# Kernel tuning notes

Measured on AMD Instinct MI355X. Metric: run time of the kernel, lower is better.

## Reference

```python
import jax, jax.numpy as jnp
import numpy as np

B, N = 4096, 8192
PULSE_LO = 40.0 / 60.0   # Hz
PULSE_HI = 250.0 / 60.0  # Hz


def setup_inputs() -> dict:
    key = jax.random.key(0)
    k1, k2 = jax.random.split(key)
    outputs = jax.random.normal(k1, (B, N), dtype=jnp.float32)
    # reference heart rates in Hz, uniform inside the pulse band
    targets = jax.random.uniform(k2, (B, 1), dtype=jnp.float32,
                                 minval=PULSE_LO, maxval=PULSE_HI)
    return {"outputs": outputs, "targets": targets, "Fs": 20}


def reference(outputs, targets, Fs):
    n = outputs.shape[-1]
    F = n // 2 + 1
    f = jnp.linspace(0.0, Fs / 2.0, F, dtype=jnp.float32)  # [F]

    min_idx = jnp.argmin(jnp.abs(f - PULSE_LO))
    max_idx = jnp.argmin(jnp.abs(f - PULSE_HI))

    # normalized rFFT power spectrum (torch.rfft(..., normalized=True) divides by sqrt(N))
    X = jnp.fft.rfft(outputs) * (1.0 / np.sqrt(n))          # [B, F] complex
    P1 = X.real ** 2 + X.imag ** 2                          # [B, F]

    # per-sample reference bin index
    r = jnp.argmin(jnp.abs(f[None, :] - targets.reshape(-1, 1)), axis=1)  # [B]
    rb = r[:, None]                                         # [B, 1]
    i = jnp.arange(F)[None, :]                              # [1, F]

    # signal mask u: 1 at ref and 1st harmonic, 0.5 at ref+-1 (applied after, as in torch)
    u = jnp.where((i == rb - 1) | (i == rb + 1), 0.5,
                  jnp.where((i == rb) | (i == 2 * rb), 1.0, 0.0))
    # noise mask w = 1 - u, zeroed outside pulse band and around 1st harmonic
    w = jnp.where((i < min_idx) | (i >= max_idx) |
                  (i == 2 * rb - 1) | (i == 2 * rb + 1),
                  0.0, 1.0 - u)

    signal_energy = jnp.sum(P1 * u, axis=1)                 # [B]
    noise_energy = jnp.sum(P1 * w, axis=1)                  # [B]
    losses = -10.0 * jnp.log(signal_energy / (noise_energy + 1.0)) / jnp.log(10.0)
    return jnp.mean(losses)
```

## Files before the change

### kernel.cpp

```cpp
#include <hip/hip_runtime.h>
#include <math.h>

#define NC 4096
#define TPB 256

__device__ __forceinline__ float2 cmul(float2 a, float2 b) {
    return make_float2(a.x * b.x - a.y * b.y, a.x * b.y + a.y * b.x);
}

__global__ __launch_bounds__(TPB) void snr_kernel(const float* __restrict__ x,
                                                  const float* __restrict__ targets,
                                                  float* __restrict__ out) {
    __shared__ __align__(16) float2 A[NC];
    __shared__ __align__(16) float2 Bf[NC];
    const int tid = threadIdx.x;
    const int blk = blockIdx.x;

    const float4* row4 = (const float4*)(x + (size_t)blk * 8192);
    float4* A4 = (float4*)A;
#pragma unroll
    for (int k = 0; k < 8; ++k) A4[tid + k * TPB] = row4[tid + k * TPB];
    __syncthreads();

    float2* src = A;
    float2* dst = Bf;
    int n = NC;
    int ls = 0;
#pragma unroll
    for (int stage = 0; stage < 6; ++stage) {
        const float th = -6.283185307179586f / (float)n;
#pragma unroll
        for (int it = 0; it < 4; ++it) {
            const int b = tid + it * TPB;
            const int p = b >> ls;
            const int q = b - (p << ls);
            float2 a  = src[b];
            float2 bb = src[b + 1024];
            float2 c  = src[b + 2048];
            float2 d  = src[b + 3072];
            float2 apc = make_float2(a.x + c.x, a.y + c.y);
            float2 amc = make_float2(a.x - c.x, a.y - c.y);
            float2 bpd = make_float2(bb.x + d.x, bb.y + d.y);
            float2 bmd = make_float2(bb.x - d.x, bb.y - d.y);
            float ang = th * (float)p;
            float sn, cs;
            __sincosf(ang, &sn, &cs);
            float2 w1 = make_float2(cs, sn);
            float2 w2 = cmul(w1, w1);
            float2 w3 = cmul(w2, w1);
            float2 o0 = make_float2(apc.x + bpd.x, apc.y + bpd.y);
            float2 o1 = cmul(make_float2(amc.x + bmd.y, amc.y - bmd.x), w1);
            float2 o2 = cmul(make_float2(apc.x - bpd.x, apc.y - bpd.y), w2);
            float2 o3 = cmul(make_float2(amc.x - bmd.y, amc.y + bmd.x), w3);
            const int s = 1 << ls;
            const int ob = q + (p << (ls + 2));
            dst[ob]         = o0;
            dst[ob + s]     = o1;
            dst[ob + 2 * s] = o2;
            dst[ob + 3 * s] = o3;
        }
        __syncthreads();
        float2* tmp = src; src = dst; dst = tmp;
        n >>= 2;
        ls += 2;
    }

    float* P = (float*)Bf;
    for (int k = tid; k <= NC; k += TPB) {
        float2 Zk = A[k & (NC - 1)];
        float2 Zn = A[(NC - k) & (NC - 1)];
        float sx = Zk.x + Zn.x, sy = Zk.y - Zn.y;
        float dx = Zk.x - Zn.x, dy = Zk.y + Zn.y;
        float ang = -3.14159265358979323846f * (float)k * (1.0f / 4096.0f);
        float sn, cs;
        __sincosf(ang, &sn, &cs);
        float tx = dx * cs - dy * sn;
        float ty = dx * sn + dy * cs;
        float Xr = 0.5f * (sx + ty);
        float Xi = 0.5f * (sy - tx);
        P[k] = (Xr * Xr + Xi * Xi) * (1.0f / 8192.0f);
    }
    __syncthreads();

    float part = 0.0f;
    for (int i = 273 + tid; i < 1707; i += TPB) part += P[i];
#pragma unroll
    for (int off = 32; off > 0; off >>= 1) part += __shfl_down(part, off);
    float* red = (float*)A;
    const int lane = tid & 63, wid = tid >> 6;
    if (lane == 0) red[wid] = part;
    __syncthreads();

    if (tid == 0) {
        float band = red[0] + red[1] + red[2] + red[3];
        float t = targets[blk];
        const float df = 0.00244140625f;
        int c0 = (int)(t * 409.6f) - 2;
        if (c0 < 0) c0 = 0;
        int r = c0;
        float best = fabsf(df * (float)c0 - t);
        for (int i = c0 + 1; i <= c0 + 4 && i <= 4096; ++i) {
            float dd = fabsf(df * (float)i - t);
            if (dd < best) { best = dd; r = i; }
        }
        float S = P[r] + P[2 * r] + 0.5f * (P[r - 1] + P[r + 1]);
        float noise = band;
        if (r <= 1706) noise -= P[r];
        if (r - 1 >= 273) noise -= 0.5f * P[r - 1];
        if (r + 1 <= 1706) noise -= 0.5f * P[r + 1];
        if (2 * r - 1 <= 1706) noise -= P[2 * r - 1];
        if (2 * r     <= 1706) noise -= P[2 * r];
        if (2 * r + 1 <= 1706) noise -= P[2 * r + 1];
        float loss = -10.0f * log10f(S / (noise + 1.0f));
        atomicAdd(out, loss * (1.0f / 4096.0f));
    }
}

extern "C" void kernel_launch(void* const* d_in, const int* in_sizes, int n_in,
                              void* d_out, int out_size, void* d_ws, size_t ws_size,
                              hipStream_t stream) {
    const float* x = (const float*)d_in[0];
    const float* tg = (const float*)d_in[1];
    float* out = (float*)d_out;
    hipMemsetAsync(out, 0, sizeof(float), stream);
    snr_kernel<<<4096, TPB, 0, stream>>>(x, tg, out);
}
```

Measured before the change: 237.4 us.

## Replace radix-4 shared-memory FFT with register radix-16 three-pass FFT

The six radix-4 stages that ping-ponged through shared memory become three radix-16 passes computed in registers, with twiddles built from one sincos per thread and shared-memory transposes between passes. Storage moves to split real/imag arrays with an XOR swizzle to avoid bank conflicts. The post-processing now accumulates the band energy and captures the six needed bins directly, so the full power spectrum is never written. This cuts shared-memory traffic and barriers, at the cost of higher register pressure (16 complex values per thread) and twiddles generated by recurrence.

```diff
diff --git a/kernel.cpp b/kernel.cpp
--- a/kernel.cpp
+++ b/kernel.cpp
@@ -1,116 +1,173 @@
 #include <hip/hip_runtime.h>
 #include <math.h>
 
-#define NC 4096
 #define TPB 256
+#define NCX 4096
 
 __device__ __forceinline__ float2 cmul(float2 a, float2 b) {
     return make_float2(a.x * b.x - a.y * b.y, a.x * b.y + a.y * b.x);
 }
 
-__global__ __launch_bounds__(TPB) void snr_kernel(const float* __restrict__ x,
-                                                  const float* __restrict__ targets,
-                                                  float* __restrict__ out) {
-    __shared__ __align__(16) float2 A[NC];
-    __shared__ __align__(16) float2 Bf[NC];
-    const int tid = threadIdx.x;
+__device__ __forceinline__ int sw(int i) { return i ^ ((i >> 5) & 31); }
+
+__device__ __forceinline__ void dft4(float2& a, float2& b, float2& c, float2& d) {
+    float2 t0 = make_float2(a.x + c.x, a.y + c.y);
+    float2 t1 = make_float2(a.x - c.x, a.y - c.y);
+    float2 t2 = make_float2(b.x + d.x, b.y + d.y);
+    float2 t3 = make_float2(b.x - d.x, b.y - d.y);
+    a = make_float2(t0.x + t2.x, t0.y + t2.y);
+    b = make_float2(t1.x + t3.y, t1.y - t3.x);
+    c = make_float2(t0.x - t2.x, t0.y - t2.y);
+    d = make_float2(t1.x - t3.y, t1.y + t3.x);
+}
+
+__device__ __forceinline__ void dft16(float2 v[16]) {
+#pragma unroll
+    for (int j = 0; j < 4; ++j) dft4(v[j], v[4 + j], v[8 + j], v[12 + j]);
+    const float C1 = 0.9238795325112867f, S1 = 0.3826834323650898f;
+    const float R2 = 0.7071067811865476f;
+    v[5]  = cmul(v[5],  make_float2( C1, -S1));
+    v[9]  = cmul(v[9],  make_float2( R2, -R2));
+    v[13] = cmul(v[13], make_float2( S1, -C1));
+    v[6]  = cmul(v[6],  make_float2( R2, -R2));
+    v[10] = cmul(v[10], make_float2(0.f, -1.f));
+    v[14] = cmul(v[14], make_float2(-R2, -R2));
+    v[7]  = cmul(v[7],  make_float2( S1, -C1));
+    v[11] = cmul(v[11], make_float2(-R2, -R2));
+    v[15] = cmul(v[15], make_float2(-C1,  S1));
+#pragma unroll
+    for (int b = 0; b < 4; ++b) dft4(v[4 * b], v[4 * b + 1], v[4 * b + 2], v[4 * b + 3]);
+}
+
+__global__ __launch_bounds__(TPB, 4) void snr_kernel(const float* __restrict__ x,
+                                                     const float* __restrict__ targets,
+                                                     float* __restrict__ out) {
+    __shared__ float re[NCX];
+    __shared__ float im[NCX];
+    __shared__ float spec[6];
+    __shared__ float red[4];
+    __shared__ int r_sh;
+
+    const int t = threadIdx.x;
     const int blk = blockIdx.x;
 
-    const float4* row4 = (const float4*)(x + (size_t)blk * 8192);
-    float4* A4 = (float4*)A;
-#pragma unroll
-    for (int k = 0; k < 8; ++k) A4[tid + k * TPB] = row4[tid + k * TPB];
-    __syncthreads();
-
-    float2* src = A;
-    float2* dst = Bf;
-    int n = NC;
-    int ls = 0;
-#pragma unroll
-    for (int stage = 0; stage < 6; ++stage) {
-        const float th = -6.283185307179586f / (float)n;
-#pragma unroll
-        for (int it = 0; it < 4; ++it) {
-            const int b = tid + it * TPB;
-            const int p = b >> ls;
-            const int q = b - (p << ls);
-            float2 a  = src[b];
-            float2 bb = src[b + 1024];
-            float2 c  = src[b + 2048];
-            float2 d  = src[b + 3072];
-            float2 apc = make_float2(a.x + c.x, a.y + c.y);
-            float2 amc = make_float2(a.x - c.x, a.y - c.y);
-            float2 bpd = make_float2(bb.x + d.x, bb.y + d.y);
-            float2 bmd = make_float2(bb.x - d.x, bb.y - d.y);
-            float ang = th * (float)p;
-            float sn, cs;
-            __sincosf(ang, &sn, &cs);
-            float2 w1 = make_float2(cs, sn);
-            float2 w2 = cmul(w1, w1);
-            float2 w3 = cmul(w2, w1);
-            float2 o0 = make_float2(apc.x + bpd.x, apc.y + bpd.y);
-            float2 o1 = cmul(make_float2(amc.x + bmd.y, amc.y - bmd.x), w1);
-            float2 o2 = cmul(make_float2(apc.x - bpd.x, apc.y - bpd.y), w2);
-            float2 o3 = cmul(make_float2(amc.x - bmd.y, amc.y + bmd.x), w3);
-            const int s = 1 << ls;
-            const int ob = q + (p << (ls + 2));
-            dst[ob]         = o0;
-            dst[ob + s]     = o1;
-            dst[ob + 2 * s] = o2;
-            dst[ob + 3 * s] = o3;
+    if (t == 0) {
+        float tg = targets[blk];
+        const float df = 0.00244140625f;
+        int c0 = (int)(tg * 409.6f) - 2;
+        if (c0 < 0) c0 = 0;
+        int r = c0;
+        float best = fabsf(df * (float)c0 - tg);
+        for (int i = c0 + 1; i <= c0 + 4 && i <= 4096; ++i) {
+            float dd = fabsf(df * (float)i - tg);
+            if (dd < best) { best = dd; r = i; }
         }
-        __syncthreads();
-        float2* tmp = src; src = dst; dst = tmp;
-        n >>= 2;
-        ls += 2;
+        r_sh = r;
     }
 
-    float* P = (float*)Bf;
-    for (int k = tid; k <= NC; k += TPB) {
-        float2 Zk = A[k & (NC - 1)];
-        float2 Zn = A[(NC - k) & (NC - 1)];
-        float sx = Zk.x + Zn.x, sy = Zk.y - Zn.y;
-        float dx = Zk.x - Zn.x, dy = Zk.y + Zn.y;
-        float ang = -3.14159265358979323846f * (float)k * (1.0f / 4096.0f);
-        float sn, cs;
-        __sincosf(ang, &sn, &cs);
-        float tx = dx * cs - dy * sn;
-        float ty = dx * sn + dy * cs;
-        float Xr = 0.5f * (sx + ty);
-        float Xi = 0.5f * (sy - tx);
-        P[k] = (Xr * Xr + Xi * Xi) * (1.0f / 8192.0f);
+    float2 v[16];
+    const float2* row = (const float2*)(x + (size_t)blk * 8192);
+#pragma unroll
+    for (int l = 0; l < 16; ++l) v[l] = row[t + 256 * l];
+
+    dft16(v);
+    {
+        float ang = -1.5339807878856412e-3f * (float)t;
+        float sn, cs; __sincosf(ang, &sn, &cs);
+        float2 w1 = make_float2(cs, sn);
+        float2 w2 = cmul(w1, w1), w3 = cmul(w2, w1);
+        float2 w4 = cmul(w2, w2), w8 = cmul(w4, w4), w12 = cmul(w8, w4);
+        float2 wa[4] = {make_float2(1.f, 0.f), w1, w2, w3};
+        float2 wb[4] = {make_float2(1.f, 0.f), w4, w8, w12};
+#pragma unroll
+        for (int m = 0; m < 16; ++m) {
+            float2 y = cmul(v[4 * (m & 3) + (m >> 2)], cmul(wb[m >> 2], wa[m & 3]));
+            int idx = sw(16 * t + m);
+            re[idx] = y.x; im[idx] = y.y;
+        }
     }
     __syncthreads();
 
-    float part = 0.0f;
-    for (int i = 273 + tid; i < 1707; i += TPB) part += P[i];
 #pragma unroll
-    for (int off = 32; off > 0; off >>= 1) part += __shfl_down(part, off);
-    float* red = (float*)A;
-    const int lane = tid & 63, wid = tid >> 6;
-    if (lane == 0) red[wid] = part;
+    for (int l = 0; l < 16; ++l) { int idx = sw(t + 256 * l); v[l] = make_float2(re[idx], im[idx]); }
+    __syncthreads();
+    dft16(v);
+    {
+        const int p = t >> 4, q = t & 15;
+        float ang = -0.02454369260617026f * (float)p;
+        float sn, cs; __sincosf(ang, &sn, &cs);
+        float2 w1 = make_float2(cs, sn);
+        float2 w2 = cmul(w1, w1), w3 = cmul(w2, w1);
+        float2 w4 = cmul(w2, w2), w8 = cmul(w4, w4), w12 = cmul(w8, w4);
+        float2 wa[4] = {make_float2(1.f, 0.f), w1, w2, w3};
+        float2 wb[4] = {make_float2(1.f, 0.f), w4, w8, w12};
+#pragma unroll
+        for (int m = 0; m < 16; ++m) {
+            float2 y = cmul(v[4 * (m & 3) + (m >> 2)], cmul(wb[m >> 2], wa[m & 3]));
+            int idx = sw(q + 256 * p + 16 * m);
+            re[idx] = y.x; im[idx] = y.y;
+        }
+    }
     __syncthreads();
 
-    if (tid == 0) {
-        float band = red[0] + red[1] + red[2] + red[3];
-        float t = targets[blk];
-        const float df = 0.00244140625f;
-        int c0 = (int)(t * 409.6f) - 2;
-        if (c0 < 0) c0 = 0;
-        int r = c0;
-        float best = fabsf(df * (float)c0 - t);
-        for (int i = c0 + 1; i <= c0 + 4 && i <= 4096; ++i) {
-            float dd = fabsf(df * (float)i - t);
-            if (dd < best) { best = dd; r = i; }
+#pragma unroll
+    for (int l = 0; l < 16; ++l) { int idx = sw(t + 256 * l); v[l] = make_float2(re[idx], im[idx]); }
+    __syncthreads();
+    dft16(v);
+#pragma unroll
+    for (int m = 0; m < 16; ++m) {
+        float2 y = v[4 * (m & 3) + (m >> 2)];
+        int idx = sw(t + 256 * m);
+        re[idx] = y.x; im[idx] = y.y;
+    }
+    __syncthreads();
+
+    const int r = r_sh;
+    const int r2 = 2 * r;
+    float band = 0.f;
+    {
+        float ang = -7.669903939428206e-4f * (float)t;
+        float sn, cs; __sincosf(ang, &sn, &cs);
+        float2 wk = make_float2(cs, sn);
+        const float2 wstep = make_float2(0.9807852804032304f, -0.19509032201612825f);
+#pragma unroll
+        for (int m = 0; m < 16; ++m) {
+            int k = t + 256 * m;
+            int i1 = sw(k);
+            int i2 = sw((4096 - k) & 4095);
+            float2 Zk = make_float2(re[i1], im[i1]);
+            float2 Zn = make_float2(re[i2], im[i2]);
+            float sx = Zk.x + Zn.x, sy = Zk.y - Zn.y;
+            float dx = Zk.x - Zn.x, dy = Zk.y + Zn.y;
+            float tx = dx * wk.x - dy * wk.y;
+            float ty = dx * wk.y + dy * wk.x;
+            float Xr = 0.5f * (sx + ty);
+            float Xi = 0.5f * (sy - tx);
+            float P = (Xr * Xr + Xi * Xi) * (1.0f / 8192.0f);
+            if ((unsigned)(k - 273) <= 1433u) band += P;
+            int d1 = k - (r - 1);
+            if ((unsigned)d1 < 3u) spec[d1] = P;
+            int d2 = k - (r2 - 1);
+            if ((unsigned)d2 < 3u) spec[3 + d2] = P;
+            wk = cmul(wk, wstep);
         }
-        float S = P[r] + P[2 * r] + 0.5f * (P[r - 1] + P[r + 1]);
-        float noise = band;
-        if (r <= 1706) noise -= P[r];
-        if (r - 1 >= 273) noise -= 0.5f * P[r - 1];
-        if (r + 1 <= 1706) noise -= 0.5f * P[r + 1];
-        if (2 * r - 1 <= 1706) noise -= P[2 * r - 1];
-        if (2 * r     <= 1706) noise -= P[2 * r];
-        if (2 * r + 1 <= 1706) noise -= P[2 * r + 1];
+    }
+
+#pragma unroll
+    for (int off = 32; off > 0; off >>= 1) band += __shfl_down(band, off);
+    if ((t & 63) == 0) red[t >> 6] = band;
+    __syncthreads();
+
+    if (t == 0) {
+        float bb = red[0] + red[1] + red[2] + red[3];
+        float S = spec[1] + spec[4] + 0.5f * (spec[0] + spec[2]);
+        float noise = bb;
+        if (r <= 1706)      noise -= spec[1];
+        if (r - 1 >= 273)   noise -= 0.5f * spec[0];
+        if (r + 1 <= 1706)  noise -= 0.5f * spec[2];
+        if (r2 - 1 <= 1706) noise -= spec[3];
+        if (r2 <= 1706)     noise -= spec[4];
+        if (r2 + 1 <= 1706) noise -= spec[5];
         float loss = -10.0f * log10f(S / (noise + 1.0f));
         atomicAdd(out, loss * (1.0f / 4096.0f));
     }
```

Result: faster. 214.4 us (-9.7%).
